# Kernel tuning notes

Hardware: AMD Instinct MI355X
Metric: run time of the kernel (lower is better)

## Reference

```python
import jax, jax.numpy as jnp
import numpy as np

BLOCK = 128          # block_size in the source
FP8_MAX = 448.0      # max representable magnitude of float8_e4m3fn


def _quant_weight(w):
    """Pre-quantize a [N, K] float weight into fp8 values + per 128x128 block scales."""
    N, K = w.shape
    wb = w.reshape(N // BLOCK, BLOCK, K // BLOCK, BLOCK)
    w_scale = jnp.max(jnp.abs(wb), axis=(1, 3)) / FP8_MAX           # [Nb, Kb]
    s = jnp.where(w_scale == 0, 1.0, w_scale)
    wq = (wb / s[:, None, :, None]).astype(jnp.float8_e4m3fn).astype(jnp.float32)
    return wq.reshape(N, K), w_scale


def setup_inputs() -> dict:
    key = jax.random.key(0)
    kx, kw = jax.random.split(key)
    M, K, N = 16384, 2048, 2048
    x = jax.random.normal(kx, (M, K), dtype=jnp.float32)
    w = jax.random.normal(kw, (N, K), dtype=jnp.float32) * 0.02
    w_fp8, w_scale = _quant_weight(w)
    return {"x": x, "w_fp8": w_fp8, "w_scale": w_scale}


def reference(x, w_fp8, w_scale):
    """fp8 block-quantized linear: act_quant(x) then dequantized GEMM.

    x:       [M, K] float32 activations
    w_fp8:   [N, K] fp8-valued weight (stored as float32, exactly e4m3 representable)
    w_scale: [N/128, K/128] per-block weight scales
    """
    M, K = x.shape
    N = w_fp8.shape[0]
    # --- act_quant: per 128-element block along K, scale = amax / 448 ---
    xb = x.reshape(M, K // BLOCK, BLOCK)
    x_scale = jnp.max(jnp.abs(xb), axis=-1) / FP8_MAX               # [M, Kb]
    sx = jnp.where(x_scale == 0, 1.0, x_scale)
    xq = (xb / sx[..., None]).astype(jnp.float8_e4m3fn).astype(jnp.float32)
    # --- fp8_gemm with inline dequant: scales factor out per (m-block, n-block, k-block)
    # sum_kb sx[m,kb]*sw[nb,kb]*(xq . wq) == (xq*sx) @ (wq*sw)^T exactly ---
    x_deq = (xq * sx[..., None]).reshape(M, K)
    w_deq = (w_fp8.reshape(N // BLOCK, BLOCK, K // BLOCK, BLOCK)
             * w_scale[:, None, :, None]).reshape(N, K)
    return x_deq @ w_deq.T                                          # [M, N]
```

## Files before the change

kernel.cpp:

```cpp
#include <hip/hip_runtime.h>

#define M_DIM 16384
#define N_DIM 2048
#define K_DIM 2048
#define KB    (K_DIM / 128)
#define BM 128
#define BN 128
#define BK 64

#define XGRID (M_DIM * K_DIM / 1024)
#define WGRID (N_DIM * K_DIM / 1024)

typedef __bf16 bf16x8 __attribute__((ext_vector_type(8)));
typedef float  f32x4  __attribute__((ext_vector_type(4)));

__device__ __forceinline__ unsigned short f32_to_bf16_rne(float f) {
    unsigned int u = __float_as_uint(f);
    u += 0x7FFFu + ((u >> 16) & 1u);
    return (unsigned short)(u >> 16);
}

__global__ __launch_bounds__(256) void quant_all_kernel(const float* __restrict__ x,
                                                        unsigned short* __restrict__ xdq,
                                                        const float* __restrict__ w,
                                                        const float* __restrict__ wscale,
                                                        unsigned short* __restrict__ wdq) {
    const int tid = threadIdx.x;
    if (blockIdx.x < XGRID) {
        const size_t base = ((size_t)blockIdx.x * 256 + tid) * 4;
        const float4 v = *(const float4*)(x + base);
        float amax = fmaxf(fmaxf(fabsf(v.x), fabsf(v.y)), fmaxf(fabsf(v.z), fabsf(v.w)));
#pragma unroll
        for (int m = 16; m >= 1; m >>= 1)
            amax = fmaxf(amax, __shfl_xor(amax, m, 64));
        float s = amax / 448.0f;
        if (s == 0.0f) s = 1.0f;
        const int p01 = __builtin_amdgcn_cvt_pk_fp8_f32(v.x / s, v.y / s, 0, false);
        const int p23 = __builtin_amdgcn_cvt_pk_fp8_f32(v.z / s, v.w / s, 0, false);
        const float d0 = __builtin_amdgcn_cvt_f32_fp8(p01, 0) * s;
        const float d1 = __builtin_amdgcn_cvt_f32_fp8(p01, 1) * s;
        const float d2 = __builtin_amdgcn_cvt_f32_fp8(p23, 0) * s;
        const float d3 = __builtin_amdgcn_cvt_f32_fp8(p23, 1) * s;
        uint2 out;
        out.x = (unsigned int)f32_to_bf16_rne(d0) | ((unsigned int)f32_to_bf16_rne(d1) << 16);
        out.y = (unsigned int)f32_to_bf16_rne(d2) | ((unsigned int)f32_to_bf16_rne(d3) << 16);
        *(uint2*)(xdq + base) = out;
    } else {
        const size_t e = ((size_t)(blockIdx.x - XGRID) * 256 + tid) * 4;
        const float4 v = *(const float4*)(w + e);
        const int n = (int)(e >> 11);
        const int k = (int)(e & 2047);
        const float s = wscale[(n >> 7) * KB + (k >> 7)];
        uint2 out;
        out.x = (unsigned int)f32_to_bf16_rne(v.x * s) | ((unsigned int)f32_to_bf16_rne(v.y * s) << 16);
        out.y = (unsigned int)f32_to_bf16_rne(v.z * s) | ((unsigned int)f32_to_bf16_rne(v.w * s) << 16);
        *(uint2*)(wdq + e) = out;
    }
}

__global__ __launch_bounds__(256) void gemm_bt_kernel(const unsigned short* __restrict__ A,
                                                      const unsigned short* __restrict__ B,
                                                      float* __restrict__ C) {
    __shared__ __align__(16) unsigned short As[BM * BK];
    __shared__ __align__(16) unsigned short Bs[BN * BK];

    const int tid  = threadIdx.x;
    const int lane = tid & 63;
    const int wave = tid >> 6;
    const int wm   = (wave >> 1) * 64;
    const int wn   = (wave & 1) * 64;
    const int quad = lane >> 4;
    const int l16  = lane & 15;

    const int m0 = blockIdx.x * BM;
    const int n0 = blockIdx.y * BN;

    f32x4 acc[4][4] = {};

    const int srow = tid >> 3;
    const int scol = (tid & 7) ^ (srow & 7);
    const unsigned short* gA = A + (size_t)(m0 + srow) * K_DIM + scol * 8;
    const unsigned short* gB = B + (size_t)(n0 + srow) * K_DIM + scol * 8;

    for (int kt = 0; kt < K_DIM / BK; ++kt) {
        const int k0 = kt * BK;
#pragma unroll
        for (int i = 0; i < 4; ++i) {
            __builtin_amdgcn_global_load_lds(
                (__attribute__((address_space(1))) void*)(gA + (size_t)(i * 32) * K_DIM + k0),
                (__attribute__((address_space(3))) void*)(As + (i * 256 + wave * 64) * 8),
                16, 0, 0);
        }
#pragma unroll
        for (int i = 0; i < 4; ++i) {
            __builtin_amdgcn_global_load_lds(
                (__attribute__((address_space(1))) void*)(gB + (size_t)(i * 32) * K_DIM + k0),
                (__attribute__((address_space(3))) void*)(Bs + (i * 256 + wave * 64) * 8),
                16, 0, 0);
        }
        __syncthreads();
#pragma unroll
        for (int ks = 0; ks < BK; ks += 32) {
            const int c = (ks >> 3) + quad;
            const int swz = (c ^ (l16 & 7)) * 8;
            bf16x8 af[4], bfr[4];
#pragma unroll
            for (int i = 0; i < 4; ++i)
                af[i] = *(const bf16x8*)(As + (wm + i * 16 + l16) * BK + swz);
#pragma unroll
            for (int j = 0; j < 4; ++j)
                bfr[j] = *(const bf16x8*)(Bs + (wn + j * 16 + l16) * BK + swz);
#pragma unroll
            for (int i = 0; i < 4; ++i)
#pragma unroll
                for (int j = 0; j < 4; ++j)
                    acc[i][j] = __builtin_amdgcn_mfma_f32_16x16x32_bf16(af[i], bfr[j], acc[i][j], 0, 0, 0);
        }
        __syncthreads();
    }

#pragma unroll
    for (int i = 0; i < 4; ++i) {
        const int row = m0 + wm + i * 16 + quad * 4;
#pragma unroll
        for (int j = 0; j < 4; ++j) {
            const int col = n0 + wn + j * 16 + l16;
            float* cp = C + (size_t)row * N_DIM + col;
#pragma unroll
            for (int r = 0; r < 4; ++r)
                cp[(size_t)r * N_DIM] = acc[i][j][r];
        }
    }
}

extern "C" void kernel_launch(void* const* d_in, const int* in_sizes, int n_in,
                              void* d_out, int out_size, void* d_ws, size_t ws_size,
                              hipStream_t stream) {
    const float* x      = (const float*)d_in[0];
    const float* wfp8   = (const float*)d_in[1];
    const float* wscale = (const float*)d_in[2];
    float* out = (float*)d_out;

    unsigned short* xdq = (unsigned short*)d_ws;
    unsigned short* wdq = xdq + (size_t)M_DIM * K_DIM;

    quant_all_kernel<<<XGRID + WGRID, 256, 0, stream>>>(x, xdq, wfp8, wscale, wdq);
    gemm_bt_kernel<<<dim3(M_DIM / BM, N_DIM / BN), 256, 0, stream>>>(xdq, wdq, out);
}
```

Before: 372.1 us.

## Enlarge GEMM tile to 256x256 with double-buffered LDS and phased prefetch

Grows the block tile to 256x256 with 512 threads (8 waves, each computing 128x64) and double-buffers the LDS tiles. The next K-tile's direct-to-LDS global loads are interleaved across four MFMA phases, with explicit vmcnt waits, raw barriers and setprio. The goal is to overlap global memory latency with MFMA work and raise arithmetic intensity per block. In exchange it uses more LDS (128KB) and more accumulator registers. The hand-tuned waitcnt and barrier ordering is fragile and could race or stall if the counts are wrong.

After: 380.7 us. +2.3%, slower.

```diff
diff --git a/kernel.cpp b/kernel.cpp
--- a/kernel.cpp
+++ b/kernel.cpp
@@ -4,9 +4,11 @@
 #define N_DIM 2048
 #define K_DIM 2048
 #define KB    (K_DIM / 128)
-#define BM 128
-#define BN 128
+
+#define BM 256
+#define BN 256
 #define BK 64
+#define NT (K_DIM / BK)
 
 #define XGRID (M_DIM * K_DIM / 1024)
 #define WGRID (N_DIM * K_DIM / 1024)
@@ -58,69 +60,100 @@
     }
 }
 
-__global__ __launch_bounds__(256) void gemm_bt_kernel(const unsigned short* __restrict__ A,
-                                                      const unsigned short* __restrict__ B,
-                                                      float* __restrict__ C) {
-    __shared__ __align__(16) unsigned short As[BM * BK];
-    __shared__ __align__(16) unsigned short Bs[BN * BK];
+__global__ __launch_bounds__(512, 2) void gemm_bt_kernel(const unsigned short* __restrict__ A,
+                                                         const unsigned short* __restrict__ B,
+                                                         float* __restrict__ C) {
+    __shared__ __align__(16) unsigned short As[2][BM * BK];
+    __shared__ __align__(16) unsigned short Bs[2][BN * BK];
 
     const int tid  = threadIdx.x;
     const int lane = tid & 63;
     const int wave = tid >> 6;
-    const int wm   = (wave >> 1) * 64;
-    const int wn   = (wave & 1) * 64;
+    const int wm   = (wave >> 2) * 128;
+    const int wn   = (wave & 3) * 64;
     const int quad = lane >> 4;
     const int l16  = lane & 15;
 
     const int m0 = blockIdx.x * BM;
     const int n0 = blockIdx.y * BN;
 
-    f32x4 acc[4][4] = {};
+    f32x4 acc[8][4] = {};
 
     const int srow = tid >> 3;
     const int scol = (tid & 7) ^ (srow & 7);
     const unsigned short* gA = A + (size_t)(m0 + srow) * K_DIM + scol * 8;
     const unsigned short* gB = B + (size_t)(n0 + srow) * K_DIM + scol * 8;
 
-    for (int kt = 0; kt < K_DIM / BK; ++kt) {
-        const int k0 = kt * BK;
-#pragma unroll
-        for (int i = 0; i < 4; ++i) {
-            __builtin_amdgcn_global_load_lds(
-                (__attribute__((address_space(1))) void*)(gA + (size_t)(i * 32) * K_DIM + k0),
-                (__attribute__((address_space(3))) void*)(As + (i * 256 + wave * 64) * 8),
-                16, 0, 0);
-        }
-#pragma unroll
-        for (int i = 0; i < 4; ++i) {
-            __builtin_amdgcn_global_load_lds(
-                (__attribute__((address_space(1))) void*)(gB + (size_t)(i * 32) * K_DIM + k0),
-                (__attribute__((address_space(3))) void*)(Bs + (i * 256 + wave * 64) * 8),
-                16, 0, 0);
-        }
-        __syncthreads();
-#pragma unroll
-        for (int ks = 0; ks < BK; ks += 32) {
-            const int c = (ks >> 3) + quad;
-            const int swz = (c ^ (l16 & 7)) * 8;
-            bf16x8 af[4], bfr[4];
-#pragma unroll
-            for (int i = 0; i < 4; ++i)
-                af[i] = *(const bf16x8*)(As + (wm + i * 16 + l16) * BK + swz);
-#pragma unroll
-            for (int j = 0; j < 4; ++j)
-                bfr[j] = *(const bf16x8*)(Bs + (wn + j * 16 + l16) * BK + swz);
-#pragma unroll
-            for (int i = 0; i < 4; ++i)
-#pragma unroll
-                for (int j = 0; j < 4; ++j)
-                    acc[i][j] = __builtin_amdgcn_mfma_f32_16x16x32_bf16(af[i], bfr[j], acc[i][j], 0, 0, 0);
-        }
-        __syncthreads();
+#define STAGE_A(NXT, i, ktn) \
+    __builtin_amdgcn_global_load_lds( \
+        (__attribute__((address_space(1))) void*)(gA + (size_t)((i) * 64) * K_DIM + (ktn) * BK), \
+        (__attribute__((address_space(3))) void*)(&As[NXT][(i) * 4096 + wave * 512]), 16, 0, 0)
+#define STAGE_B(NXT, i, ktn) \
+    __builtin_amdgcn_global_load_lds( \
+        (__attribute__((address_space(1))) void*)(gB + (size_t)((i) * 64) * K_DIM + (ktn) * BK), \
+        (__attribute__((address_space(3))) void*)(&Bs[NXT][(i) * 4096 + wave * 512]), 16, 0, 0)
+
+#define VMCNT(n) asm volatile("s_waitcnt vmcnt(" #n ")" ::: "memory")
+
+#define PHASE(CUR, MI0, NJ0, WAIT, ...) do { \
+    bf16x8 af[4][2], bfr[2][2]; \
+    _Pragma("unroll") \
+    for (int i = 0; i < 4; ++i) { \
+      _Pragma("unroll") \
+      for (int kk = 0; kk < 2; ++kk) \
+        af[i][kk] = *(const bf16x8*)(&As[CUR][(wm + ((MI0) + i) * 16 + l16) * BK + ((kk * 4 + quad) ^ (l16 & 7)) * 8]); \
+    } \
+    _Pragma("unroll") \
+    for (int j = 0; j < 2; ++j) { \
+      _Pragma("unroll") \
+      for (int kk = 0; kk < 2; ++kk) \
+        bfr[j][kk] = *(const bf16x8*)(&Bs[CUR][(wn + ((NJ0) + j) * 16 + l16) * BK + ((kk * 4 + quad) ^ (l16 & 7)) * 8]); \
+    } \
+    __VA_ARGS__; \
+    __builtin_amdgcn_s_barrier(); \
+    asm volatile("s_waitcnt lgkmcnt(0)" ::: "memory"); \
+    __builtin_amdgcn_s_setprio(1); \
+    _Pragma("unroll") \
+    for (int i = 0; i < 4; ++i) { \
+      _Pragma("unroll") \
+      for (int j = 0; j < 2; ++j) { \
+        acc[(MI0) + i][(NJ0) + j] = __builtin_amdgcn_mfma_f32_16x16x32_bf16(af[i][0], bfr[j][0], acc[(MI0) + i][(NJ0) + j], 0, 0, 0); \
+        acc[(MI0) + i][(NJ0) + j] = __builtin_amdgcn_mfma_f32_16x16x32_bf16(af[i][1], bfr[j][1], acc[(MI0) + i][(NJ0) + j], 0, 0, 0); \
+      } \
+    } \
+    __builtin_amdgcn_s_setprio(0); \
+    WAIT; \
+    __builtin_amdgcn_s_barrier(); \
+  } while (0)
+
+#define TILE_FULL(CUR, NXT, KTN) do { \
+    PHASE(CUR, 0, 0, (void)0, STAGE_B(NXT, 0, KTN); STAGE_B(NXT, 1, KTN); STAGE_B(NXT, 2, KTN)); \
+    PHASE(CUR, 0, 2, VMCNT(6), STAGE_B(NXT, 3, KTN); STAGE_A(NXT, 0, KTN); STAGE_A(NXT, 2, KTN)); \
+    PHASE(CUR, 4, 0, (void)0, STAGE_A(NXT, 1, KTN); STAGE_A(NXT, 3, KTN)); \
+    PHASE(CUR, 4, 2, VMCNT(2), (void)0); \
+  } while (0)
+
+#define TILE_LAST(CUR) do { \
+    PHASE(CUR, 0, 0, (void)0, (void)0); \
+    PHASE(CUR, 0, 2, VMCNT(0), (void)0); \
+    PHASE(CUR, 4, 0, (void)0, (void)0); \
+    PHASE(CUR, 4, 2, (void)0, (void)0); \
+  } while (0)
+
+    STAGE_B(0, 0, 0); STAGE_B(0, 1, 0); STAGE_B(0, 2, 0); STAGE_B(0, 3, 0);
+    STAGE_A(0, 0, 0); STAGE_A(0, 2, 0); STAGE_A(0, 1, 0); STAGE_A(0, 3, 0);
+    VMCNT(2);
+    __builtin_amdgcn_s_barrier();
+
+    for (int kt = 0; kt < NT - 2; kt += 2) {
+        TILE_FULL(0, 1, kt + 1);
+        TILE_FULL(1, 0, kt + 2);
     }
+    TILE_FULL(0, 1, NT - 1);
+    TILE_LAST(1);
 
 #pragma unroll
-    for (int i = 0; i < 4; ++i) {
+    for (int i = 0; i < 8; ++i) {
         const int row = m0 + wm + i * 16 + quad * 4;
 #pragma unroll
         for (int j = 0; j < 4; ++j) {
@@ -145,5 +178,5 @@
     unsigned short* wdq = xdq + (size_t)M_DIM * K_DIM;
 
     quant_all_kernel<<<XGRID + WGRID, 256, 0, stream>>>(x, xdq, wfp8, wscale, wdq);
-    gemm_bt_kernel<<<dim3(M_DIM / BM, N_DIM / BN), 256, 0, stream>>>(xdq, wdq, out);
+    gemm_bt_kernel<<<dim3(M_DIM / BM, N_DIM / BN), 512, 0, stream>>>(xdq, wdq, out);
 }
```
